# Kernel optimization log

Measured on AMD Instinct MI355X. Metric: run time of the kernel, lower is better.

## Reference

```python
import jax, jax.numpy as jnp
import numpy as np

N = 50000          # nodes
E = 1_600_000      # edges (avg degree 32)
D = 128            # input_dim
H = 128            # hidden_dim
EPS = 1e-5


def setup_inputs() -> dict:
    key = jax.random.key(0)
    ks = jax.random.split(key, 8)
    x = jax.random.normal(ks[0], (N, D), jnp.float32)
    edge_index = jax.random.randint(ks[1], (2, E), 0, N)
    message = jax.random.normal(ks[2], (E, H), jnp.float32)

    def lin(k, fin, fout):
        return jax.random.normal(k, (fin, fout), jnp.float32) / np.sqrt(fin).astype(np.float32)

    return {
        "x": x,
        "message": message,
        "W1": lin(ks[3], D + 2 * H, H), "b1": jnp.zeros((H,), jnp.float32),
        "g1": jnp.ones((H,), jnp.float32), "be1": jnp.zeros((H,), jnp.float32),
        "W2": lin(ks[4], H, H), "b2": jnp.zeros((H,), jnp.float32),
        "g2": jnp.ones((H,), jnp.float32), "be2": jnp.zeros((H,), jnp.float32),
        "Wa": lin(ks[5], H, 1), "ba": jnp.zeros((1,), jnp.float32),
        "edge_index": edge_index,
    }


def _batchnorm(h, g, b):
    # training-mode BatchNorm1d: biased batch stats over the node dim
    mu = h.mean(axis=0)
    var = h.var(axis=0)
    return (h - mu) * jax.lax.rsqrt(var + EPS) * g + b


def reference(x, message, W1, b1, g1, be1, W2, b2, g2, be2, Wa, ba, edge_index):
    row, col = edge_index[0], edge_index[1]
    n = x.shape[0]

    def smax(idx):
        m = jax.ops.segment_max(message, idx, num_segments=n)  # [N, H]
        # torch_scatter scatter(reduce='max') leaves empty slots at 0
        return jnp.where(jnp.isfinite(m), m, jnp.zeros_like(m))

    fwd = smax(col)
    bwd = smax(row)
    out = jnp.concatenate([x, fwd, bwd], axis=1)  # [N, D+2H]

    h = jax.nn.relu(_batchnorm(out @ W1 + b1, g1, be1))  # dropout = identity (eval)
    h = jax.nn.relu(_batchnorm(h @ W2 + b2, g2, be2))
    att = jax.nn.sigmoid(h @ Wa + ba).reshape(-1)        # [N]
    return h, att
```

## Files before the change

### kernel.cpp

```cpp
#include <hip/hip_runtime.h>
#include <math.h>

#define N_NODES 50000
#define N_EDGES 1600000
#define DIM 128
#define EPS 1e-5f
#define CAP 128

typedef short bf16x8 __attribute__((ext_vector_type(8)));
typedef float f32x4 __attribute__((ext_vector_type(4)));
typedef unsigned short ushort_t;

__device__ __forceinline__ float4 f4max(float4 a, float4 b) {
    return make_float4(fmaxf(a.x, b.x), fmaxf(a.y, b.y), fmaxf(a.z, b.z), fmaxf(a.w, b.w));
}

__device__ __forceinline__ ushort_t f2bf(float f) {
    unsigned int u = __float_as_uint(f);
    return (ushort_t)((u + 0x7FFFu + ((u >> 16) & 1u)) >> 16);
}

__global__ __launch_bounds__(256) void k_init(float* __restrict__ stats, int* __restrict__ cnt) {
    int i = blockIdx.x * 256 + threadIdx.x;
    if (i < 512) stats[i] = 0.0f;
    if (i < 2 * N_NODES) cnt[i] = 0;
}

__global__ __launch_bounds__(256) void k_prep(const float* __restrict__ W1, const float* __restrict__ W2,
                                              ushort_t* __restrict__ W1t, ushort_t* __restrict__ W2t) {
    int gid = blockIdx.x * 256 + threadIdx.x;
    if (gid < 128 * 384) {
        int j = gid / 384, k = gid % 384;
        W1t[gid] = f2bf(W1[k * 128 + j]);
    } else {
        int g2 = gid - 128 * 384;
        if (g2 < 128 * 128) {
            int j = g2 / 128, k = g2 % 128;
            W2t[g2] = f2bf(W2[k * 128 + j]);
        }
    }
}

__global__ __launch_bounds__(256) void k_bucket(const int* __restrict__ ei, int* __restrict__ cnt,
                                                int* __restrict__ slots) {
    int t = blockIdx.x * 256 + threadIdx.x;
    if (t >= N_EDGES / 4) return;
    int4 r4 = reinterpret_cast<const int4*>(ei)[t];
    int4 c4 = reinterpret_cast<const int4*>(ei + N_EDGES)[t];
    int e = t * 4;
    slots[c4.x * CAP + atomicAdd(&cnt[c4.x], 1)] = e + 0;
    slots[c4.y * CAP + atomicAdd(&cnt[c4.y], 1)] = e + 1;
    slots[c4.z * CAP + atomicAdd(&cnt[c4.z], 1)] = e + 2;
    slots[c4.w * CAP + atomicAdd(&cnt[c4.w], 1)] = e + 3;
    slots[(N_NODES + r4.x) * CAP + atomicAdd(&cnt[N_NODES + r4.x], 1)] = e + 0;
    slots[(N_NODES + r4.y) * CAP + atomicAdd(&cnt[N_NODES + r4.y], 1)] = e + 1;
    slots[(N_NODES + r4.z) * CAP + atomicAdd(&cnt[N_NODES + r4.z], 1)] = e + 2;
    slots[(N_NODES + r4.w) * CAP + atomicAdd(&cnt[N_NODES + r4.w], 1)] = e + 3;
}

__global__ __launch_bounds__(256) void k_gather(const float4* __restrict__ msgv,
                                                const int* __restrict__ slots,
                                                const int* __restrict__ cnt,
                                                float* __restrict__ fwd,
                                                float* __restrict__ bwd) {
    const int wid = blockIdx.x * 4 + (threadIdx.x >> 6);
    const int dir = (wid >= N_NODES);
    const int n = dir ? wid - N_NODES : wid;
    const int lane = threadIdx.x & 63;
    const int q = lane & 31;
    const int h = lane >> 5;
    const int c = cnt[dir * N_NODES + n];
    const int* el = slots + (size_t)(dir * N_NODES + n) * CAP;

    float4 acc = make_float4(-INFINITY, -INFINITY, -INFINITY, -INFINITY);
    const int nfull = c >> 2;
    for (int g = h; g < nfull; g += 2) {
        int4 e4 = *reinterpret_cast<const int4*>(el + g * 4);
        float4 m0 = msgv[(size_t)e4.x * 32 + q];
        float4 m1 = msgv[(size_t)e4.y * 32 + q];
        float4 m2 = msgv[(size_t)e4.z * 32 + q];
        float4 m3 = msgv[(size_t)e4.w * 32 + q];
        acc = f4max(acc, f4max(f4max(m0, m1), f4max(m2, m3)));
    }
    if (h == (nfull & 1)) {
        for (int p = nfull * 4; p < c; ++p) {
            acc = f4max(acc, msgv[(size_t)el[p] * 32 + q]);
        }
    }
    acc.x = fmaxf(acc.x, __shfl_xor(acc.x, 32));
    acc.y = fmaxf(acc.y, __shfl_xor(acc.y, 32));
    acc.z = fmaxf(acc.z, __shfl_xor(acc.z, 32));
    acc.w = fmaxf(acc.w, __shfl_xor(acc.w, 32));

    if (h == 0) {
        if (c == 0) acc = make_float4(0.0f, 0.0f, 0.0f, 0.0f);
        float* dst = dir ? bwd : fwd;
        reinterpret_cast<float4*>(dst + n * DIM)[q] = acc;
    }
}


__global__ __launch_bounds__(256) void k_gemm1(const float* __restrict__ x,
                                               const float* __restrict__ fwd,
                                               const float* __restrict__ bwd,
                                               const ushort_t* __restrict__ W1t,
                                               const float* __restrict__ b1,
                                               float* __restrict__ h1p,
                                               float* __restrict__ stats) {
    __shared__ uint4 rowsA4[512];
    __shared__ uint4 Wt4[1024];
    __shared__ float bias[128];
    __shared__ float s_sum[128], s_sq[128];
    char* rowsA = (char*)rowsA4;
    char* Wt = (char*)Wt4;

    const int tid = threadIdx.x;
    const int wid = tid >> 6;
    const int lane = tid & 63;
    const int ln15 = lane & 15;
    const int kb16 = (lane >> 4) * 16;
    const int n0 = blockIdx.x * 64;
    const int rA = wid * 16 + ln15;
    const int rsw = (rA & 7) << 4;

    if (tid < 128) { bias[tid] = b1[tid]; s_sum[tid] = 0.0f; s_sq[tid] = 0.0f; }

    f32x4 acc[8];
#pragma unroll
    for (int i = 0; i < 8; ++i) acc[i] = (f32x4){0.0f, 0.0f, 0.0f, 0.0f};

    for (int c = 0; c < 6; ++c) {
        const float* src = (c < 2) ? x : ((c < 4) ? fwd : bwd);
        const int koff = (c & 1) * 64;
        __syncthreads();
#pragma unroll
        for (int i = 0; i < 2; ++i) {
            int g = tid + i * 256;
            int r = g >> 3, k8 = g & 7;
            int n = n0 + r;
            float4 v0 = make_float4(0.f, 0.f, 0.f, 0.f), v1 = v0;
            if (n < N_NODES) {
                const float4* p = reinterpret_cast<const float4*>(src + n * DIM + koff + k8 * 8);
                v0 = p[0]; v1 = p[1];
            }
            ushort_t pk[8] = {f2bf(v0.x), f2bf(v0.y), f2bf(v0.z), f2bf(v0.w),
                              f2bf(v1.x), f2bf(v1.y), f2bf(v1.z), f2bf(v1.w)};
            *(uint4*)(rowsA + ((r * 128 + k8 * 16) ^ ((r & 7) << 4))) = *(const uint4*)pk;
        }
#pragma unroll
        for (int i = 0; i < 4; ++i) {
            int g = tid + i * 256;
            int j = g >> 3, k8 = g & 7;
            uint4 w = *reinterpret_cast<const uint4*>(W1t + j * 384 + c * 64 + k8 * 8);
            *(uint4*)(Wt + ((j * 128 + k8 * 16) ^ ((j & 7) << 4))) = w;
        }
        __syncthreads();
#pragma unroll
        for (int ks = 0; ks < 2; ++ks) {
            bf16x8 a = *(bf16x8*)(rowsA + ((rA * 128 + ks * 64 + kb16) ^ rsw));
#pragma unroll
            for (int ct = 0; ct < 8; ++ct) {
                int j = ct * 16 + ln15;
                bf16x8 b = *(bf16x8*)(Wt + ((j * 128 + ks * 64 + kb16) ^ ((j & 7) << 4)));
                acc[ct] = __builtin_amdgcn_mfma_f32_16x16x32_bf16(a, b, acc[ct], 0, 0, 0);
            }
        }
    }
    __syncthreads();
    const int jcol = ln15;
#pragma unroll
    for (int ct = 0; ct < 8; ++ct) {
        int j = ct * 16 + jcol;
        float bj = bias[j];
        float s = 0.0f, q = 0.0f;
#pragma unroll
        for (int r = 0; r < 4; ++r) {
            int n = n0 + wid * 16 + (lane >> 4) * 4 + r;
            if (n < N_NODES) {
                float v = acc[ct][r] + bj;
                h1p[n * DIM + j] = v;
                s += v; q += v * v;
            }
        }
        s += __shfl_xor(s, 16); s += __shfl_xor(s, 32);
        q += __shfl_xor(q, 16); q += __shfl_xor(q, 32);
        if ((lane >> 4) == 0) { atomicAdd(&s_sum[j], s); atomicAdd(&s_sq[j], q); }
    }
    __syncthreads();
    if (tid < 128) {
        atomicAdd(&stats[tid], s_sum[tid]);
        atomicAdd(&stats[128 + tid], s_sq[tid]);
    }
}

__global__ __launch_bounds__(256) void k_gemm2(const float* __restrict__ h1p,
                                               const ushort_t* __restrict__ W2t,
                                               const float* __restrict__ b2,
                                               const float* __restrict__ g1,
                                               const float* __restrict__ be1,
                                               float* __restrict__ h2p,
                                               float* __restrict__ stats) {
    __shared__ uint4 rowsA4[512];
    __shared__ uint4 Wt4[1024];
    __shared__ float bias[128];
    __shared__ float ssc[128], ssh[128];
    __shared__ float s_sum[128], s_sq[128];
    char* rowsA = (char*)rowsA4;
    char* Wt = (char*)Wt4;

    const int tid = threadIdx.x;
    const int wid = tid >> 6;
    const int lane = tid & 63;
    const int ln15 = lane & 15;
    const int kb16 = (lane >> 4) * 16;
    const int n0 = blockIdx.x * 64;
    const int rA = wid * 16 + ln15;
    const int rsw = (rA & 7) << 4;

    if (tid < 128) {
        float mu = stats[tid] * (1.0f / N_NODES);
        float var = stats[128 + tid] * (1.0f / N_NODES) - mu * mu;
        float sc = rsqrtf(var + EPS) * g1[tid];
        ssc[tid] = sc;
        ssh[tid] = be1[tid] - mu * sc;
        bias[tid] = b2[tid];
        s_sum[tid] = 0.0f; s_sq[tid] = 0.0f;
    }

    f32x4 acc[8];
#pragma unroll
    for (int i = 0; i < 8; ++i) acc[i] = (f32x4){0.0f, 0.0f, 0.0f, 0.0f};

    for (int c = 0; c < 2; ++c) {
        const int koff = c * 64;
        __syncthreads();
#pragma unroll
        for (int i = 0; i < 2; ++i) {
            int g = tid + i * 256;
            int r = g >> 3, k8 = g & 7;
            int n = n0 + r;
            float4 v0 = make_float4(0.f, 0.f, 0.f, 0.f), v1 = v0;
            if (n < N_NODES) {
                const float4* p = reinterpret_cast<const float4*>(h1p + n * DIM + koff + k8 * 8);
                float4 c0 = reinterpret_cast<const float4*>(ssc + koff + k8 * 8)[0];
                float4 c1 = reinterpret_cast<const float4*>(ssc + koff + k8 * 8)[1];
                float4 h0 = reinterpret_cast<const float4*>(ssh + koff + k8 * 8)[0];
                float4 h1 = reinterpret_cast<const float4*>(ssh + koff + k8 * 8)[1];
                v0 = p[0]; v1 = p[1];
                v0.x = fmaxf(v0.x * c0.x + h0.x, 0.f); v0.y = fmaxf(v0.y * c0.y + h0.y, 0.f);
                v0.z = fmaxf(v0.z * c0.z + h0.z, 0.f); v0.w = fmaxf(v0.w * c0.w + h0.w, 0.f);
                v1.x = fmaxf(v1.x * c1.x + h1.x, 0.f); v1.y = fmaxf(v1.y * c1.y + h1.y, 0.f);
                v1.z = fmaxf(v1.z * c1.z + h1.z, 0.f); v1.w = fmaxf(v1.w * c1.w + h1.w, 0.f);
            }
            ushort_t pk[8] = {f2bf(v0.x), f2bf(v0.y), f2bf(v0.z), f2bf(v0.w),
                              f2bf(v1.x), f2bf(v1.y), f2bf(v1.z), f2bf(v1.w)};
            *(uint4*)(rowsA + ((r * 128 + k8 * 16) ^ ((r & 7) << 4))) = *(const uint4*)pk;
        }
#pragma unroll
        for (int i = 0; i < 4; ++i) {
            int g = tid + i * 256;
            int j = g >> 3, k8 = g & 7;
            uint4 w = *reinterpret_cast<const uint4*>(W2t + j * 128 + c * 64 + k8 * 8);
            *(uint4*)(Wt + ((j * 128 + k8 * 16) ^ ((j & 7) << 4))) = w;
        }
        __syncthreads();
#pragma unroll
        for (int ks = 0; ks < 2; ++ks) {
            bf16x8 a = *(bf16x8*)(rowsA + ((rA * 128 + ks * 64 + kb16) ^ rsw));
#pragma unroll
            for (int ct = 0; ct < 8; ++ct) {
                int j = ct * 16 + ln15;
                bf16x8 b = *(bf16x8*)(Wt + ((j * 128 + ks * 64 + kb16) ^ ((j & 7) << 4)));
                acc[ct] = __builtin_amdgcn_mfma_f32_16x16x32_bf16(a, b, acc[ct], 0, 0, 0);
            }
        }
    }
    __syncthreads();
    const int jcol = ln15;
#pragma unroll
    for (int ct = 0; ct < 8; ++ct) {
        int j = ct * 16 + jcol;
        float bj = bias[j];
        float s = 0.0f, q = 0.0f;
#pragma unroll
        for (int r = 0; r < 4; ++r) {
            int n = n0 + wid * 16 + (lane >> 4) * 4 + r;
            if (n < N_NODES) {
                float v = acc[ct][r] + bj;
                h2p[n * DIM + j] = v;
                s += v; q += v * v;
            }
        }
        s += __shfl_xor(s, 16); s += __shfl_xor(s, 32);
        q += __shfl_xor(q, 16); q += __shfl_xor(q, 32);
        if ((lane >> 4) == 0) { atomicAdd(&s_sum[j], s); atomicAdd(&s_sq[j], q); }
    }
    __syncthreads();
    if (tid < 128) {
        atomicAdd(&stats[256 + tid], s_sum[tid]);
        atomicAdd(&stats[384 + tid], s_sq[tid]);
    }
}

__global__ __launch_bounds__(256) void k_final(const float* __restrict__ h2p,
                                               const float* __restrict__ stats,
                                               const float* __restrict__ g2,
                                               const float* __restrict__ be2,
                                               const float* __restrict__ Wa,
                                               const float* __restrict__ ba,
                                               float* __restrict__ out) {
    const int lane = threadIdx.x & 63;
    const int wv = threadIdx.x >> 6;
    const int n = blockIdx.x * 4 + wv;
    if (n >= N_NODES) return;
    const int j0 = lane, j1 = lane + 64;

    float mu0 = stats[256 + j0] * (1.0f / N_NODES);
    float var0 = stats[384 + j0] * (1.0f / N_NODES) - mu0 * mu0;
    float sc0 = rsqrtf(var0 + EPS) * g2[j0];
    float sh0 = be2[j0] - mu0 * sc0;
    float mu1 = stats[256 + j1] * (1.0f / N_NODES);
    float var1 = stats[384 + j1] * (1.0f / N_NODES) - mu1 * mu1;
    float sc1 = rsqrtf(var1 + EPS) * g2[j1];
    float sh1 = be2[j1] - mu1 * sc1;

    float v0 = fmaxf(h2p[n * DIM + j0] * sc0 + sh0, 0.0f);
    float v1 = fmaxf(h2p[n * DIM + j1] * sc1 + sh1, 0.0f);
    out[n * DIM + j0] = v0;
    out[n * DIM + j1] = v1;

    float p = v0 * Wa[j0] + v1 * Wa[j1];
#pragma unroll
    for (int off = 32; off > 0; off >>= 1) p += __shfl_down(p, off);
    if (lane == 0) out[N_NODES * DIM + n] = 1.0f / (1.0f + expf(-(p + ba[0])));
}

extern "C" void kernel_launch(void* const* d_in, const int* in_sizes, int n_in,
                              void* d_out, int out_size, void* d_ws, size_t ws_size,
                              hipStream_t stream) {
    const float* x   = (const float*)d_in[0];
    const float* msg = (const float*)d_in[1];
    const float* W1  = (const float*)d_in[2];
    const float* b1  = (const float*)d_in[3];
    const float* g1  = (const float*)d_in[4];
    const float* be1 = (const float*)d_in[5];
    const float* W2  = (const float*)d_in[6];
    const float* b2  = (const float*)d_in[7];
    const float* g2  = (const float*)d_in[8];
    const float* be2 = (const float*)d_in[9];
    const float* Wa  = (const float*)d_in[10];
    const float* ba  = (const float*)d_in[11];
    const int*   ei  = (const int*)d_in[12];

    float*    ws    = (float*)d_ws;
    float*    stats = ws;
    float*    fwd   = ws + 512;
    float*    bwd   = fwd + N_NODES * DIM;
    int*      cnt   = (int*)(bwd + N_NODES * DIM);
    int*      slots = cnt + 2 * N_NODES;
    ushort_t* W1t   = (ushort_t*)(slots + 2 * N_NODES * CAP);
    ushort_t* W2t   = W1t + 128 * 384;

    float* h1p = (float*)d_out;
    float* h2p = fwd;
    float* out = (float*)d_out;

    k_init<<<(2 * N_NODES + 255) / 256, 256, 0, stream>>>(stats, cnt);
    k_prep<<<(128 * 384 + 128 * 128 + 255) / 256, 256, 0, stream>>>(W1, W2, W1t, W2t);
    k_bucket<<<(N_EDGES / 4 + 255) / 256, 256, 0, stream>>>(ei, cnt, slots);
    k_gather<<<(2 * N_NODES) / 4, 256, 0, stream>>>((const float4*)msg, slots, cnt, fwd, bwd);
    k_gemm1<<<(N_NODES + 63) / 64, 256, 0, stream>>>(x, fwd, bwd, W1t, b1, h1p, stats);
    k_gemm2<<<(N_NODES + 63) / 64, 256, 0, stream>>>(h1p, W2t, b2, g1, be1, h2p, stats);
    k_final<<<(N_NODES + 3) / 4, 256, 0, stream>>>(h2p, stats, g2, be2, Wa, ba, out);
}
```

Before: 684.5 us.

## Store intermediates in bf16, unroll gather with nontemporal loads, shrink slot capacity

The fwd/bwd segment-max results and the pre-BN hidden activations h1/h2 are now stored as bf16 instead of fp32, which halves intermediate write and read traffic between the gather and GEMM kernels. BN statistics are still accumulated in fp32 from the unrounded values. The gather loop is unrolled to eight message loads per iteration with two accumulators and nontemporal loads, the init kernel is replaced by memsets, and the per-node slot capacity drops from 128 to 96. The capacity cut risks overflow on high-degree nodes, and normalizing bf16-rounded h values against fp32 stats adds a small precision error.

```diff
diff --git a/kernel.cpp b/kernel.cpp
--- a/kernel.cpp
+++ b/kernel.cpp
@@ -5,25 +5,26 @@
 #define N_EDGES 1600000
 #define DIM 128
 #define EPS 1e-5f
-#define CAP 128
+#define CAP 96
 
 typedef short bf16x8 __attribute__((ext_vector_type(8)));
 typedef float f32x4 __attribute__((ext_vector_type(4)));
+typedef int i32x4 __attribute__((ext_vector_type(4)));
 typedef unsigned short ushort_t;
 
-__device__ __forceinline__ float4 f4max(float4 a, float4 b) {
-    return make_float4(fmaxf(a.x, b.x), fmaxf(a.y, b.y), fmaxf(a.z, b.z), fmaxf(a.w, b.w));
+__device__ __forceinline__ f32x4 v4max(f32x4 a, f32x4 b) {
+    f32x4 r;
+    r[0] = fmaxf(a[0], b[0]); r[1] = fmaxf(a[1], b[1]);
+    r[2] = fmaxf(a[2], b[2]); r[3] = fmaxf(a[3], b[3]);
+    return r;
 }
 
 __device__ __forceinline__ ushort_t f2bf(float f) {
     unsigned int u = __float_as_uint(f);
     return (ushort_t)((u + 0x7FFFu + ((u >> 16) & 1u)) >> 16);
 }
-
-__global__ __launch_bounds__(256) void k_init(float* __restrict__ stats, int* __restrict__ cnt) {
-    int i = blockIdx.x * 256 + threadIdx.x;
-    if (i < 512) stats[i] = 0.0f;
-    if (i < 2 * N_NODES) cnt[i] = 0;
+__device__ __forceinline__ float bf2f(ushort_t u) {
+    return __uint_as_float(((unsigned int)u) << 16);
 }
 
 __global__ __launch_bounds__(256) void k_prep(const float* __restrict__ W1, const float* __restrict__ W2,
@@ -58,11 +59,11 @@
     slots[(N_NODES + r4.w) * CAP + atomicAdd(&cnt[N_NODES + r4.w], 1)] = e + 3;
 }
 
-__global__ __launch_bounds__(256) void k_gather(const float4* __restrict__ msgv,
+__global__ __launch_bounds__(256) void k_gather(const f32x4* __restrict__ msgv,
                                                 const int* __restrict__ slots,
                                                 const int* __restrict__ cnt,
-                                                float* __restrict__ fwd,
-                                                float* __restrict__ bwd) {
+                                                ushort_t* __restrict__ fwd,
+                                                ushort_t* __restrict__ bwd) {
     const int wid = blockIdx.x * 4 + (threadIdx.x >> 6);
     const int dir = (wid >= N_NODES);
     const int n = dir ? wid - N_NODES : wid;
@@ -72,40 +73,58 @@
     const int c = cnt[dir * N_NODES + n];
     const int* el = slots + (size_t)(dir * N_NODES + n) * CAP;
 
-    float4 acc = make_float4(-INFINITY, -INFINITY, -INFINITY, -INFINITY);
+    f32x4 acc0 = {-INFINITY, -INFINITY, -INFINITY, -INFINITY};
+    f32x4 acc1 = acc0;
     const int nfull = c >> 2;
-    for (int g = h; g < nfull; g += 2) {
-        int4 e4 = *reinterpret_cast<const int4*>(el + g * 4);
-        float4 m0 = msgv[(size_t)e4.x * 32 + q];
-        float4 m1 = msgv[(size_t)e4.y * 32 + q];
-        float4 m2 = msgv[(size_t)e4.z * 32 + q];
-        float4 m3 = msgv[(size_t)e4.w * 32 + q];
-        acc = f4max(acc, f4max(f4max(m0, m1), f4max(m2, m3)));
+    int g = h;
+    for (; g + 2 < nfull; g += 4) {
+        i32x4 ea = *reinterpret_cast<const i32x4*>(el + g * 4);
+        i32x4 eb = *reinterpret_cast<const i32x4*>(el + (g + 2) * 4);
+        f32x4 m0 = __builtin_nontemporal_load(&msgv[(size_t)ea[0] * 32 + q]);
+        f32x4 m1 = __builtin_nontemporal_load(&msgv[(size_t)ea[1] * 32 + q]);
+        f32x4 m2 = __builtin_nontemporal_load(&msgv[(size_t)ea[2] * 32 + q]);
+        f32x4 m3 = __builtin_nontemporal_load(&msgv[(size_t)ea[3] * 32 + q]);
+        f32x4 m4 = __builtin_nontemporal_load(&msgv[(size_t)eb[0] * 32 + q]);
+        f32x4 m5 = __builtin_nontemporal_load(&msgv[(size_t)eb[1] * 32 + q]);
+        f32x4 m6 = __builtin_nontemporal_load(&msgv[(size_t)eb[2] * 32 + q]);
+        f32x4 m7 = __builtin_nontemporal_load(&msgv[(size_t)eb[3] * 32 + q]);
+        acc0 = v4max(acc0, v4max(v4max(m0, m1), v4max(m2, m3)));
+        acc1 = v4max(acc1, v4max(v4max(m4, m5), v4max(m6, m7)));
+    }
+    for (; g < nfull; g += 2) {
+        i32x4 e4 = *reinterpret_cast<const i32x4*>(el + g * 4);
+        f32x4 m0 = __builtin_nontemporal_load(&msgv[(size_t)e4[0] * 32 + q]);
+        f32x4 m1 = __builtin_nontemporal_load(&msgv[(size_t)e4[1] * 32 + q]);
+        f32x4 m2 = __builtin_nontemporal_load(&msgv[(size_t)e4[2] * 32 + q]);
+        f32x4 m3 = __builtin_nontemporal_load(&msgv[(size_t)e4[3] * 32 + q]);
+        acc0 = v4max(acc0, v4max(v4max(m0, m1), v4max(m2, m3)));
     }
     if (h == (nfull & 1)) {
         for (int p = nfull * 4; p < c; ++p) {
-            acc = f4max(acc, msgv[(size_t)el[p] * 32 + q]);
-        }
-    }
-    acc.x = fmaxf(acc.x, __shfl_xor(acc.x, 32));
-    acc.y = fmaxf(acc.y, __shfl_xor(acc.y, 32));
-    acc.z = fmaxf(acc.z, __shfl_xor(acc.z, 32));
-    acc.w = fmaxf(acc.w, __shfl_xor(acc.w, 32));
+            acc1 = v4max(acc1, __builtin_nontemporal_load(&msgv[(size_t)el[p] * 32 + q]));
+        }
+    }
+    f32x4 acc = v4max(acc0, acc1);
+    acc[0] = fmaxf(acc[0], __shfl_xor(acc[0], 32));
+    acc[1] = fmaxf(acc[1], __shfl_xor(acc[1], 32));
+    acc[2] = fmaxf(acc[2], __shfl_xor(acc[2], 32));
+    acc[3] = fmaxf(acc[3], __shfl_xor(acc[3], 32));
 
     if (h == 0) {
-        if (c == 0) acc = make_float4(0.0f, 0.0f, 0.0f, 0.0f);
-        float* dst = dir ? bwd : fwd;
-        reinterpret_cast<float4*>(dst + n * DIM)[q] = acc;
+        if (c == 0) { acc[0] = 0.f; acc[1] = 0.f; acc[2] = 0.f; acc[3] = 0.f; }
+        ushort_t pk[4] = {f2bf(acc[0]), f2bf(acc[1]), f2bf(acc[2]), f2bf(acc[3])};
+        ushort_t* dst = (dir ? bwd : fwd) + n * DIM + q * 4;
+        *reinterpret_cast<uint2*>(dst) = *reinterpret_cast<const uint2*>(pk);
     }
 }
 
 
 __global__ __launch_bounds__(256) void k_gemm1(const float* __restrict__ x,
-                                               const float* __restrict__ fwd,
-                                               const float* __restrict__ bwd,
+                                               const ushort_t* __restrict__ fwd,
+                                               const ushort_t* __restrict__ bwd,
                                                const ushort_t* __restrict__ W1t,
                                                const float* __restrict__ b1,
-                                               float* __restrict__ h1p,
+                                               ushort_t* __restrict__ h1b,
                                                float* __restrict__ stats) {
     __shared__ uint4 rowsA4[512];
     __shared__ uint4 Wt4[1024];
@@ -130,22 +149,35 @@
     for (int i = 0; i < 8; ++i) acc[i] = (f32x4){0.0f, 0.0f, 0.0f, 0.0f};
 
     for (int c = 0; c < 6; ++c) {
-        const float* src = (c < 2) ? x : ((c < 4) ? fwd : bwd);
         const int koff = (c & 1) * 64;
         __syncthreads();
-#pragma unroll
-        for (int i = 0; i < 2; ++i) {
-            int g = tid + i * 256;
-            int r = g >> 3, k8 = g & 7;
-            int n = n0 + r;
-            float4 v0 = make_float4(0.f, 0.f, 0.f, 0.f), v1 = v0;
-            if (n < N_NODES) {
-                const float4* p = reinterpret_cast<const float4*>(src + n * DIM + koff + k8 * 8);
-                v0 = p[0]; v1 = p[1];
-            }
-            ushort_t pk[8] = {f2bf(v0.x), f2bf(v0.y), f2bf(v0.z), f2bf(v0.w),
-                              f2bf(v1.x), f2bf(v1.y), f2bf(v1.z), f2bf(v1.w)};
-            *(uint4*)(rowsA + ((r * 128 + k8 * 16) ^ ((r & 7) << 4))) = *(const uint4*)pk;
+        if (c < 2) {
+#pragma unroll
+            for (int i = 0; i < 2; ++i) {
+                int g = tid + i * 256;
+                int r = g >> 3, k8 = g & 7;
+                int n = n0 + r;
+                f32x4 v0 = {0.f, 0.f, 0.f, 0.f}, v1 = v0;
+                if (n < N_NODES) {
+                    const f32x4* p = reinterpret_cast<const f32x4*>(x + n * DIM + koff + k8 * 8);
+                    v0 = __builtin_nontemporal_load(p);
+                    v1 = __builtin_nontemporal_load(p + 1);
+                }
+                ushort_t pk[8] = {f2bf(v0[0]), f2bf(v0[1]), f2bf(v0[2]), f2bf(v0[3]),
+                                  f2bf(v1[0]), f2bf(v1[1]), f2bf(v1[2]), f2bf(v1[3])};
+                *(uint4*)(rowsA + ((r * 128 + k8 * 16) ^ ((r & 7) << 4))) = *(const uint4*)pk;
+            }
+        } else {
+            const ushort_t* src16 = (c < 4) ? fwd : bwd;
+#pragma unroll
+            for (int i = 0; i < 2; ++i) {
+                int g = tid + i * 256;
+                int r = g >> 3, k8 = g & 7;
+                int n = n0 + r;
+                uint4 v = make_uint4(0u, 0u, 0u, 0u);
+                if (n < N_NODES) v = *reinterpret_cast<const uint4*>(src16 + n * DIM + koff + k8 * 8);
+                *(uint4*)(rowsA + ((r * 128 + k8 * 16) ^ ((r & 7) << 4))) = v;
+            }
         }
 #pragma unroll
         for (int i = 0; i < 4; ++i) {
@@ -178,7 +210,7 @@
             int n = n0 + wid * 16 + (lane >> 4) * 4 + r;
             if (n < N_NODES) {
                 float v = acc[ct][r] + bj;
-                h1p[n * DIM + j] = v;
+                h1b[n * DIM + j] = f2bf(v);
                 s += v; q += v * v;
             }
         }
@@ -193,12 +225,12 @@
     }
 }
 
-__global__ __launch_bounds__(256) void k_gemm2(const float* __restrict__ h1p,
+__global__ __launch_bounds__(256) void k_gemm2(const ushort_t* __restrict__ h1b,
                                                const ushort_t* __restrict__ W2t,
                                                const float* __restrict__ b2,
                                                const float* __restrict__ g1,
                                                const float* __restrict__ be1,
-                                               float* __restrict__ h2p,
+                                               ushort_t* __restrict__ h2b,
                                                float* __restrict__ stats) {
     __shared__ uint4 rowsA4[512];
     __shared__ uint4 Wt4[1024];
@@ -239,21 +271,17 @@
             int g = tid + i * 256;
             int r = g >> 3, k8 = g & 7;
             int n = n0 + r;
-            float4 v0 = make_float4(0.f, 0.f, 0.f, 0.f), v1 = v0;
+            ushort_t pk[8] = {0, 0, 0, 0, 0, 0, 0, 0};
             if (n < N_NODES) {
-                const float4* p = reinterpret_cast<const float4*>(h1p + n * DIM + koff + k8 * 8);
-                float4 c0 = reinterpret_cast<const float4*>(ssc + koff + k8 * 8)[0];
-                float4 c1 = reinterpret_cast<const float4*>(ssc + koff + k8 * 8)[1];
-                float4 h0 = reinterpret_cast<const float4*>(ssh + koff + k8 * 8)[0];
-                float4 h1 = reinterpret_cast<const float4*>(ssh + koff + k8 * 8)[1];
-                v0 = p[0]; v1 = p[1];
-                v0.x = fmaxf(v0.x * c0.x + h0.x, 0.f); v0.y = fmaxf(v0.y * c0.y + h0.y, 0.f);
-                v0.z = fmaxf(v0.z * c0.z + h0.z, 0.f); v0.w = fmaxf(v0.w * c0.w + h0.w, 0.f);
-                v1.x = fmaxf(v1.x * c1.x + h1.x, 0.f); v1.y = fmaxf(v1.y * c1.y + h1.y, 0.f);
-                v1.z = fmaxf(v1.z * c1.z + h1.z, 0.f); v1.w = fmaxf(v1.w * c1.w + h1.w, 0.f);
-            }
-            ushort_t pk[8] = {f2bf(v0.x), f2bf(v0.y), f2bf(v0.z), f2bf(v0.w),
-                              f2bf(v1.x), f2bf(v1.y), f2bf(v1.z), f2bf(v1.w)};
+                uint4 raw = *reinterpret_cast<const uint4*>(h1b + n * DIM + koff + k8 * 8);
+                const ushort_t* rp = (const ushort_t*)&raw;
+#pragma unroll
+                for (int t = 0; t < 8; ++t) {
+                    int kk = koff + k8 * 8 + t;
+                    float v = fmaxf(bf2f(rp[t]) * ssc[kk] + ssh[kk], 0.0f);
+                    pk[t] = f2bf(v);
+                }
+            }
             *(uint4*)(rowsA + ((r * 128 + k8 * 16) ^ ((r & 7) << 4))) = *(const uint4*)pk;
         }
 #pragma unroll
@@ -287,7 +315,7 @@
             int n = n0 + wid * 16 + (lane >> 4) * 4 + r;
             if (n < N_NODES) {
                 float v = acc[ct][r] + bj;
-                h2p[n * DIM + j] = v;
+                h2b[n * DIM + j] = f2bf(v);
                 s += v; q += v * v;
             }
         }
@@ -302,7 +330,7 @@
     }
 }
 
-__global__ __launch_bounds__(256) void k_final(const float* __restrict__ h2p,
+__global__ __launch_bounds__(256) void k_final(const ushort_t* __restrict__ h2b,
                                                const float* __restrict__ stats,
                                                const float* __restrict__ g2,
                                                const float* __restrict__ be2,
@@ -324,8 +352,8 @@
     float sc1 = rsqrtf(var1 + EPS) * g2[j1];
     float sh1 = be2[j1] - mu1 * sc1;
 
-    float v0 = fmaxf(h2p[n * DIM + j0] * sc0 + sh0, 0.0f);
-    float v1 = fmaxf(h2p[n * DIM + j1] * sc1 + sh1, 0.0f);
+    float v0 = fmaxf(bf2f(h2b[n * DIM + j0]) * sc0 + sh0, 0.0f);
+    float v1 = fmaxf(bf2f(h2b[n * DIM + j1]) * sc1 + sh1, 0.0f);
     out[n * DIM + j0] = v0;
     out[n * DIM + j1] = v1;
 
@@ -352,24 +380,24 @@
     const float* ba  = (const float*)d_in[11];
     const int*   ei  = (const int*)d_in[12];
 
-    float*    ws    = (float*)d_ws;
-    float*    stats = ws;
-    float*    fwd   = ws + 512;
-    float*    bwd   = fwd + N_NODES * DIM;
-    int*      cnt   = (int*)(bwd + N_NODES * DIM);
+    float*    stats = (float*)d_ws;
+    ushort_t* fwdb  = (ushort_t*)(stats + 512);
+    ushort_t* bwdb  = fwdb + N_NODES * DIM;
+    int*      cnt   = (int*)(bwdb + N_NODES * DIM);
     int*      slots = cnt + 2 * N_NODES;
     ushort_t* W1t   = (ushort_t*)(slots + 2 * N_NODES * CAP);
     ushort_t* W2t   = W1t + 128 * 384;
 
-    float* h1p = (float*)d_out;
-    float* h2p = fwd;
-    float* out = (float*)d_out;
-
-    k_init<<<(2 * N_NODES + 255) / 256, 256, 0, stream>>>(stats, cnt);
+    ushort_t* h1b = (ushort_t*)d_out;
+    ushort_t* h2b = fwdb;
+    float*    out = (float*)d_out;
+
+    (void)hipMemsetAsync(stats, 0, 512 * sizeof(float), stream);
+    (void)hipMemsetAsync(cnt, 0, 2 * N_NODES * sizeof(int), stream);
     k_prep<<<(128 * 384 + 128 * 128 + 255) / 256, 256, 0, stream>>>(W1, W2, W1t, W2t);
     k_bucket<<<(N_EDGES / 4 + 255) / 256, 256, 0, stream>>>(ei, cnt, slots);
-    k_gather<<<(2 * N_NODES) / 4, 256, 0, stream>>>((const float4*)msg, slots, cnt, fwd, bwd);
-    k_gemm1<<<(N_NODES + 63) / 64, 256, 0, stream>>>(x, fwd, bwd, W1t, b1, h1p, stats);
-    k_gemm2<<<(N_NODES + 63) / 64, 256, 0, stream>>>(h1p, W2t, b2, g1, be1, h2p, stats);
-    k_final<<<(N_NODES + 3) / 4, 256, 0, stream>>>(h2p, stats, g2, be2, Wa, ba, out);
-}
+    k_gather<<<(2 * N_NODES) / 4, 256, 0, stream>>>((const f32x4*)msg, slots, cnt, fwdb, bwdb);
+    k_gemm1<<<(N_NODES + 63) / 64, 256, 0, stream>>>(x, fwdb, bwdb, W1t, b1, h1b, stats);
+    k_gemm2<<<(N_NODES + 63) / 64, 256, 0, stream>>>(h1b, W2t, b2, g1, be1, h2b, stats);
+    k_final<<<(N_NODES + 3) / 4, 256, 0, stream>>>(h2b, stats, g2, be2, Wa, ba, out);
+}
```

New measurement: 621.2 us. 9.3% less time.
